# Kernel optimization log

Measured on AMD Instinct MI355X. Metric: run time of the kernel, lower is better.

## Reference

```python
import jax, jax.numpy as jnp
import numpy as np

N = 50000
E = 800000
IN_DIM = 64          # 'in_dim'; ndata h has dim 2*in_dim, p has dim in_dim
EDGE_DIM = 32
OUT_DIM = 64
AVG_D_LOG = 2.8332   # avg_d['log'] = log(avg_degree + 1), avg_degree = 16
EPS_STD = 1e-5
EPS_BN = 1e-5


def setup_inputs() -> dict:
    key = jax.random.key(0)
    ks = jax.random.split(key, 16)
    def glorot(k, fan_in, fan_out):
        lim = np.sqrt(6.0 / (fan_in + fan_out)).astype(np.float32)
        return jax.random.uniform(k, (fan_in, fan_out), jnp.float32, -lim, lim)
    d_pre_h = 2 * 2 * IN_DIM + EDGE_DIM   # 288
    d_pre_p = 2 * IN_DIM + EDGE_DIM       # 160
    d_post_h = (4 * 3 + 2) * IN_DIM       # 896
    d_post_p = (4 * 3 + 1) * IN_DIM       # 832
    return {
        "h": jax.random.normal(ks[0], (N, 2 * IN_DIM), jnp.float32),
        "p": jax.random.normal(ks[1], (N, IN_DIM), jnp.float32),
        "e": jax.random.normal(ks[2], (E, EDGE_DIM), jnp.float32),
        "src": jax.random.randint(ks[3], (E,), 0, N, jnp.int32),
        "dst": jax.random.randint(ks[4], (E,), 0, N, jnp.int32),
        "snorm_n": jax.random.uniform(ks[5], (N, 1), jnp.float32, 0.05, 1.0),
        "W_pre_h": glorot(ks[6], d_pre_h, IN_DIM),
        "b_pre_h": jnp.zeros((IN_DIM,), jnp.float32),
        "W_pre_p": glorot(ks[7], d_pre_p, IN_DIM),
        "b_pre_p": jnp.zeros((IN_DIM,), jnp.float32),
        "W_post_h": glorot(ks[8], d_post_h, OUT_DIM),
        "b_post_h": jnp.zeros((OUT_DIM,), jnp.float32),
        "W_post_p": glorot(ks[9], d_post_p, OUT_DIM),
        "b_post_p": jnp.zeros((OUT_DIM,), jnp.float32),
        "bn_gamma": jnp.ones((OUT_DIM,), jnp.float32),
        "bn_beta": jnp.zeros((OUT_DIM,), jnp.float32),
    }


def _agg_scale(msg, dst, deg):
    # msg: [E, d] edge messages reduced at dst; PNA aggregators mean/max/min/std
    degc = jnp.maximum(deg, 1.0)
    s = jax.ops.segment_sum(msg, dst, num_segments=N)
    mean = s / degc[:, None]
    sq = jax.ops.segment_sum(msg * msg, dst, num_segments=N) / degc[:, None]
    var = jax.nn.relu(sq - mean * mean)
    std = jnp.sqrt(var + EPS_STD)
    has = (deg > 0)[:, None]
    mx = jnp.where(has, jax.ops.segment_max(msg, dst, num_segments=N), 0.0)
    mn = jnp.where(has, jax.ops.segment_min(msg, dst, num_segments=N), 0.0)
    agg = jnp.concatenate([mean, mx, mn, std], axis=1)  # [N, 4d]
    logd = jnp.where(deg > 0, jnp.log(deg + 1.0), 1.0)
    amp = (logd / AVG_D_LOG)[:, None]
    att = (AVG_D_LOG / logd)[:, None]
    # scalers: identity, amplification, attenuation -> [N, 12d]
    return jnp.concatenate([agg, agg * amp, agg * att], axis=1)


def reference(h, p, e, src, dst, snorm_n,
              W_pre_h, b_pre_h, W_pre_p, b_pre_p,
              W_post_h, b_post_h, W_post_p, b_post_p,
              bn_gamma, bn_beta):
    # pretrans (1-layer MLP == linear) on concatenated edge endpoint features
    z_h = jnp.concatenate([h[src], h[dst], e], axis=1)   # [E, 4*in+edge]
    z_p = jnp.concatenate([p[src], p[dst], e], axis=1)   # [E, 2*in+edge]
    e_for_h = z_h @ W_pre_h + b_pre_h                    # [E, in]
    e_for_p = z_p @ W_pre_p + b_pre_p                    # [E, in]

    deg = jax.ops.segment_sum(jnp.ones((E,), jnp.float32), dst, num_segments=N)
    agg_h = _agg_scale(e_for_h, dst, deg)                # [N, 12*in]
    agg_p = _agg_scale(e_for_p, dst, deg)                # [N, 12*in]

    h_cat = jnp.concatenate([h, agg_h], axis=1)          # [N, 14*in]
    p_cat = jnp.concatenate([p, agg_p], axis=1)          # [N, 13*in]
    h_out = h_cat @ W_post_h + b_post_h                  # [N, out]
    p_out = p_cat @ W_post_p + b_post_p                  # [N, out]

    # graph norm
    h_out = h_out * snorm_n
    # batch norm (training-mode batch statistics, biased variance)
    mu = jnp.mean(h_out, axis=0)
    var = jnp.mean((h_out - mu) ** 2, axis=0)
    h_out = (h_out - mu) / jnp.sqrt(var + EPS_BN) * bn_gamma + bn_beta
    # dropout = identity (eval / p=0)
    return h_out, p_out
```

## Files before the change

kernel.cpp:

```cpp
#include <hip/hip_runtime.h>
#include <hip/hip_bf16.h>
#include <hip/hip_fp16.h>


#define N_NODES 50000
#define N_EDGES 800000
#define NS 3200000
#define AVG_D_LOG 2.8332f

typedef unsigned short u16;
typedef unsigned int u32;
typedef __attribute__((ext_vector_type(8))) short short8;
typedef __attribute__((ext_vector_type(4))) float f32x4;

__device__ __forceinline__ float bflo(u32 u) { return __uint_as_float(u << 16); }
__device__ __forceinline__ float bfhi(u32 u) { return __uint_as_float(u & 0xffff0000u); }
__device__ __forceinline__ float bf2f(u16 u) { return __uint_as_float(((u32)u) << 16); }
__device__ __forceinline__ u16 f2bf(float x) {
  u32 u = __float_as_uint(x);
  return (u16)((u + 0x7fff + ((u >> 16) & 1)) >> 16);
}
__device__ __forceinline__ u16 f2h(float x) { return __half_as_ushort(__float2half(x)); }
__device__ __forceinline__ float hlo(u32 u) { return __half2float(__ushort_as_half((u16)(u & 0xffffu))); }
__device__ __forceinline__ float hhi(u32 u) { return __half2float(__ushort_as_half((u16)(u >> 16))); }

__device__ __forceinline__ int is_bf(const void* gamma) {
  return ((const u32*)gamma)[0] == 0x3F803F80u ? 1 : 0;
}

__device__ __forceinline__ f32x4 mfma16(short8 a, short8 b, f32x4 c) {
  return __builtin_amdgcn_mfma_f32_16x16x32_bf16(a, b, c, 0, 0, 0);
}

__device__ __forceinline__ void load8(float z[8], const void* base, size_t off,
                                      int bf) {
  if (bf) {
    uint4 u = *(const uint4*)((const u16*)base + off);
    z[0] = bflo(u.x); z[1] = bfhi(u.x); z[2] = bflo(u.y); z[3] = bfhi(u.y);
    z[4] = bflo(u.z); z[5] = bfhi(u.z); z[6] = bflo(u.w); z[7] = bfhi(u.w);
  } else {
    const float* f = (const float*)base + off;
    float4 a = *(const float4*)f;
    float4 b = *(const float4*)(f + 4);
    z[0] = a.x; z[1] = a.y; z[2] = a.z; z[3] = a.w;
    z[4] = b.x; z[5] = b.y; z[6] = b.z; z[7] = b.w;
  }
}

__device__ __forceinline__ float load1(const void* base, size_t off, int bf) {
  return bf ? bf2f(((const u16*)base)[off]) : ((const float*)base)[off];
}

__device__ __forceinline__ short8 cvt8bf(const float z[8]) {
  union { __hip_bfloat162 b[4]; short8 s; } u;
  u.b[0] = __float22bfloat162_rn(make_float2(z[0], z[1]));
  u.b[1] = __float22bfloat162_rn(make_float2(z[2], z[3]));
  u.b[2] = __float22bfloat162_rn(make_float2(z[4], z[5]));
  u.b[3] = __float22bfloat162_rn(make_float2(z[6], z[7]));
  return u.s;
}

__global__ __launch_bounds__(256) void k_convert(
    const void* __restrict__ Wpreh, const void* __restrict__ Wprep,
    const void* __restrict__ Wposth, const void* __restrict__ Wpostp,
    const void* __restrict__ bpreh, const void* __restrict__ bprep,
    const void* __restrict__ bposth, const void* __restrict__ bpostp,
    const void* __restrict__ gamma, float* __restrict__ bias,
    u16* __restrict__ frag) {
  int i = blockIdx.x * 256 + threadIdx.x;
  if (i >= 256 + 139264) return;
  int bf = is_bf(gamma);
  if (i < 256) {
    const void* s = (i < 64) ? bpreh : (i < 128) ? bprep : (i < 192) ? bposth : bpostp;
    bias[i] = load1(s, i & 63, bf);
    return;
  }
  int g = i - 256;
  const void* W; int fidx, rowoff;
  if (g < 8192)        { W = Wpreh;  fidx = g;          rowoff = 0; }
  else if (g < 16384)  { W = Wpreh;  fidx = g - 8192;   rowoff = 128; }
  else if (g < 20480)  { W = Wprep;  fidx = g - 16384;  rowoff = 0; }
  else if (g < 24576)  { W = Wprep;  fidx = g - 20480;  rowoff = 64; }
  else if (g < 81920)  { W = Wposth; fidx = g - 24576;  rowoff = 0; }
  else if (g < 135168) { W = Wpostp; fidx = g - 81920;  rowoff = 0; }
  else if (g < 137216) { W = Wpreh;  fidx = g - 135168; rowoff = 256; }
  else                 { W = Wprep;  fidx = g - 137216; rowoff = 128; }
  int f = fidx;
  int kc = f >> 11, nt = (f >> 9) & 3, lane = (f >> 3) & 63, j = f & 7;
  int k = kc * 32 + (lane >> 4) * 8 + j;
  int n = nt * 16 + (lane & 15);
  frag[g] = f2bf(load1(W, (size_t)(rowoff + k) * 64 + n, bf));
}

__global__ __launch_bounds__(256) void k_hist(const int* __restrict__ dst,
                                              int* __restrict__ cnt) {
  int i = blockIdx.x * 256 + threadIdx.x;
  if (i < N_EDGES) atomicAdd(cnt + dst[i], 1);
}

__global__ __launch_bounds__(1024) void k_scan1(const int* __restrict__ cnt,
                                                int* __restrict__ offs,
                                                int* __restrict__ bsum) {
  __shared__ int buf[1024];
  int t = threadIdx.x;
  int i = blockIdx.x * 1024 + t;
  int v = (i < N_NODES) ? cnt[i] : 0;
  buf[t] = v;
  __syncthreads();
#pragma unroll
  for (int d = 1; d < 1024; d <<= 1) {
    int x = (t >= d) ? buf[t - d] : 0;
    __syncthreads();
    buf[t] += x;
    __syncthreads();
  }
  if (i < N_NODES) offs[i] = buf[t] - v;
  if (t == 1023) bsum[blockIdx.x] = buf[1023];
}
__global__ void k_scan2(const int* __restrict__ bsum, int* __restrict__ boff,
                        int* __restrict__ offs, int nb) {
  if (threadIdx.x == 0 && blockIdx.x == 0) {
    int run = 0;
    for (int b = 0; b < nb; ++b) { boff[b] = run; run += bsum[b]; }
    offs[N_NODES] = run;
  }
}
__global__ __launch_bounds__(256) void k_scan3(int* __restrict__ offs,
                                               const int* __restrict__ boff,
                                               int* __restrict__ cur) {
  int i = blockIdx.x * 256 + threadIdx.x;
  if (i < N_NODES) {
    int v = offs[i] + boff[i >> 10];
    offs[i] = v;
    cur[i] = v;
  }
}

__global__ __launch_bounds__(256) void k_order(const int* __restrict__ src,
                                               const int* __restrict__ dst,
                                               int* __restrict__ cur,
                                               int2* __restrict__ epack) {
  int i = blockIdx.x * 256 + threadIdx.x;
  if (i < N_EDGES) {
    int pos = atomicAdd(cur + dst[i], 1);
    epack[pos] = make_int2(i, src[i]);
  }
}

__global__ __launch_bounds__(256) void k_uproj(
    const void* __restrict__ h, const void* __restrict__ p,
    const float* __restrict__ bias, const u16* __restrict__ frag,
    const void* __restrict__ gamma, u16* __restrict__ Usrc,
    u16* __restrict__ Udst) {
  int wid = (blockIdx.x * 256 + threadIdx.x) >> 6;
  int lane = threadIdx.x & 63;
  if (wid >= 12500) return;
  int part = wid / 3125;
  int node0 = (wid % 3125) * 16;
  int bf = is_bf(gamma);
  const void* feat = (part < 2) ? h : p;
  int pitch = (part < 2) ? 128 : 64;
  int kcn = (part < 2) ? 4 : 2;
  const u16* bfr = frag + (part == 0 ? 0 : part == 1 ? 8192 : part == 2 ? 16384 : 20480);
  u16* U = (part & 1) ? Udst : Usrc;
  int tw = part >> 1;
  int m = lane & 15, quad = lane >> 4;
  f32x4 acc[4];
#pragma unroll
  for (int nt = 0; nt < 4; ++nt) acc[nt] = (f32x4){0.f, 0.f, 0.f, 0.f};
#pragma unroll
  for (int kc = 0; kc < 4; ++kc) {
    if (kc >= kcn) break;
    float z[8];
    load8(z, feat, (size_t)(node0 + m) * pitch + kc * 32 + quad * 8, bf);
    short8 a = cvt8bf(z);
#pragma unroll
    for (int nt = 0; nt < 4; ++nt) {
      short8 b = *(const short8*)(bfr + (size_t)((kc * 4 + nt) * 64 + lane) * 8);
      acc[nt] = mfma16(a, b, acc[nt]);
    }
  }
  const float* bv = (part == 1) ? bias : (part == 3) ? bias + 64 : nullptr;
#pragma unroll
  for (int r = 0; r < 4; ++r) {
    int node = node0 + quad * 4 + r;
#pragma unroll
    for (int nt = 0; nt < 4; ++nt) {
      int col = nt * 16 + m;
      float v = acc[nt][r] + (bv ? bv[col] : 0.f);
      U[(size_t)node * 128 + col * 2 + tw] = f2h(v);
    }
  }
}

template <int BF>
__global__ __launch_bounds__(256, 4) void k_aggf(
    const void* __restrict__ e, const int2* __restrict__ epack,
    const int* __restrict__ offs, const u32* __restrict__ Us32,
    const u32* __restrict__ Ud32, const u16* __restrict__ Wfh,
    const u16* __restrict__ Wfp, const void* __restrict__ gamma,
    u16* __restrict__ Ah, u16* __restrict__ Ap, float* __restrict__ degf) {
  if (is_bf(gamma) != BF) return;
  int n = blockIdx.x * 4 + (threadIdx.x >> 6);
  int lane = threadIdx.x & 63;
  if (n >= N_NODES) return;
  int m = lane & 15, quad = lane >> 4;
  int s = offs[n], epos = offs[n + 1];
  int deg = epos - s;

  short8 bh[4], bp[4];
#pragma unroll
  for (int nt = 0; nt < 4; ++nt) {
    bh[nt] = *(const short8*)(Wfh + (size_t)(nt * 64 + lane) * 8);
    bp[nt] = *(const short8*)(Wfp + (size_t)(nt * 64 + lane) * 8);
  }
  float uhd[4], upd[4];
#pragma unroll
  for (int nt = 0; nt < 4; ++nt) {
    u32 u = Ud32[(size_t)n * 64 + nt * 16 + m];
    uhd[nt] = hlo(u); upd[nt] = hhi(u);
  }
  float hsum[4], hsq[4], hmx[4], hmn[4], psum[4], psq[4], pmx[4], pmn[4];
#pragma unroll
  for (int nt = 0; nt < 4; ++nt) {
    hsum[nt] = hsq[nt] = psum[nt] = psq[nt] = 0.f;
    hmx[nt] = pmx[nt] = -3.4e38f;
    hmn[nt] = pmn[nt] = 3.4e38f;
  }

  int full = deg & ~15;
  int c0 = 0;
  for (; c0 < full; c0 += 16) {
    int eid = epack[s + c0 + m].x;
    int b0 = s + c0 + quad * 4;
    int sce0 = epack[b0].y, sce1 = epack[b0 + 1].y;
    int sce2 = epack[b0 + 2].y, sce3 = epack[b0 + 3].y;
    u32 usv0[4], usv1[4], usv2[4], usv3[4];
#pragma unroll
    for (int nt = 0; nt < 4; ++nt) {
      usv0[nt] = Us32[(size_t)sce0 * 64 + nt * 16 + m];
      usv1[nt] = Us32[(size_t)sce1 * 64 + nt * 16 + m];
      usv2[nt] = Us32[(size_t)sce2 * 64 + nt * 16 + m];
      usv3[nt] = Us32[(size_t)sce3 * 64 + nt * 16 + m];
    }
    short8 a;
    if (BF) {
      a = *(const short8*)((const u16*)e + (size_t)eid * 32 + quad * 8);
    } else {
      float z[8];
      load8(z, e, (size_t)eid * 32 + quad * 8, 0);
      a = cvt8bf(z);
    }
    {
      f32x4 acc[4];
#pragma unroll
      for (int nt = 0; nt < 4; ++nt)
        acc[nt] = mfma16(a, bh[nt], (f32x4){0.f, 0.f, 0.f, 0.f});
#pragma unroll
      for (int nt = 0; nt < 4; ++nt) {
        float w0 = acc[nt][0] + hlo(usv0[nt]);
        float w1 = acc[nt][1] + hlo(usv1[nt]);
        float w2 = acc[nt][2] + hlo(usv2[nt]);
        float w3 = acc[nt][3] + hlo(usv3[nt]);
        hmx[nt] = fmaxf(fmaxf(hmx[nt], w0), fmaxf(fmaxf(w1, w2), w3));
        hmn[nt] = fminf(fminf(hmn[nt], w0), fminf(fminf(w1, w2), w3));
        hsum[nt] += (w0 + w1) + (w2 + w3);
        hsq[nt] = fmaf(w0, w0, fmaf(w1, w1, fmaf(w2, w2, fmaf(w3, w3, hsq[nt]))));
      }
    }
    {
      f32x4 acc[4];
#pragma unroll
      for (int nt = 0; nt < 4; ++nt)
        acc[nt] = mfma16(a, bp[nt], (f32x4){0.f, 0.f, 0.f, 0.f});
#pragma unroll
      for (int nt = 0; nt < 4; ++nt) {
        float w0 = acc[nt][0] + hhi(usv0[nt]);
        float w1 = acc[nt][1] + hhi(usv1[nt]);
        float w2 = acc[nt][2] + hhi(usv2[nt]);
        float w3 = acc[nt][3] + hhi(usv3[nt]);
        pmx[nt] = fmaxf(fmaxf(pmx[nt], w0), fmaxf(fmaxf(w1, w2), w3));
        pmn[nt] = fminf(fminf(pmn[nt], w0), fminf(fminf(w1, w2), w3));
        psum[nt] += (w0 + w1) + (w2 + w3);
        psq[nt] = fmaf(w0, w0, fmaf(w1, w1, fmaf(w2, w2, fmaf(w3, w3, psq[nt]))));
      }
    }
  }
  if (c0 < deg) {
    int im = s + c0 + m; im = im < epos ? im : epos - 1;
    int eid = epack[im].x;
    int b0 = s + c0 + quad * 4;
    int i0 = b0 < epos ? b0 : epos - 1;
    int i1 = b0 + 1 < epos ? b0 + 1 : epos - 1;
    int i2 = b0 + 2 < epos ? b0 + 2 : epos - 1;
    int i3 = b0 + 3 < epos ? b0 + 3 : epos - 1;
    int sce0 = epack[i0].y, sce1 = epack[i1].y;
    int sce2 = epack[i2].y, sce3 = epack[i3].y;
    u32 usv0[4], usv1[4], usv2[4], usv3[4];
#pragma unroll
    for (int nt = 0; nt < 4; ++nt) {
      usv0[nt] = Us32[(size_t)sce0 * 64 + nt * 16 + m];
      usv1[nt] = Us32[(size_t)sce1 * 64 + nt * 16 + m];
      usv2[nt] = Us32[(size_t)sce2 * 64 + nt * 16 + m];
      usv3[nt] = Us32[(size_t)sce3 * 64 + nt * 16 + m];
    }
    short8 a;
    if (BF) {
      a = *(const short8*)((const u16*)e + (size_t)eid * 32 + quad * 8);
    } else {
      float z[8];
      load8(z, e, (size_t)eid * 32 + quad * 8, 0);
      a = cvt8bf(z);
    }
    bool v0 = (c0 + quad * 4 + 0) < deg;
    bool v1 = (c0 + quad * 4 + 1) < deg;
    bool v2 = (c0 + quad * 4 + 2) < deg;
    bool v3 = (c0 + quad * 4 + 3) < deg;
    {
      f32x4 acc[4];
#pragma unroll
      for (int nt = 0; nt < 4; ++nt)
        acc[nt] = mfma16(a, bh[nt], (f32x4){0.f, 0.f, 0.f, 0.f});
#pragma unroll
      for (int nt = 0; nt < 4; ++nt) {
        float w0 = acc[nt][0] + hlo(usv0[nt]);
        float w1 = acc[nt][1] + hlo(usv1[nt]);
        float w2 = acc[nt][2] + hlo(usv2[nt]);
        float w3 = acc[nt][3] + hlo(usv3[nt]);
        hmx[nt] = fmaxf(fmaxf(hmx[nt], w0), fmaxf(fmaxf(w1, w2), w3));
        hmn[nt] = fminf(fminf(hmn[nt], w0), fminf(fminf(w1, w2), w3));
        float z0 = v0 ? w0 : 0.f, z1 = v1 ? w1 : 0.f;
        float z2 = v2 ? w2 : 0.f, z3 = v3 ? w3 : 0.f;
        hsum[nt] += (z0 + z1) + (z2 + z3);
        hsq[nt] = fmaf(z0, z0, fmaf(z1, z1, fmaf(z2, z2, fmaf(z3, z3, hsq[nt]))));
      }
    }
    {
      f32x4 acc[4];
#pragma unroll
      for (int nt = 0; nt < 4; ++nt)
        acc[nt] = mfma16(a, bp[nt], (f32x4){0.f, 0.f, 0.f, 0.f});
#pragma unroll
      for (int nt = 0; nt < 4; ++nt) {
        float w0 = acc[nt][0] + hhi(usv0[nt]);
        float w1 = acc[nt][1] + hhi(usv1[nt]);
        float w2 = acc[nt][2] + hhi(usv2[nt]);
        float w3 = acc[nt][3] + hhi(usv3[nt]);
        pmx[nt] = fmaxf(fmaxf(pmx[nt], w0), fmaxf(fmaxf(w1, w2), w3));
        pmn[nt] = fminf(fminf(pmn[nt], w0), fminf(fminf(w1, w2), w3));
        float z0 = v0 ? w0 : 0.f, z1 = v1 ? w1 : 0.f;
        float z2 = v2 ? w2 : 0.f, z3 = v3 ? w3 : 0.f;
        psum[nt] += (z0 + z1) + (z2 + z3);
        psq[nt] = fmaf(z0, z0, fmaf(z1, z1, fmaf(z2, z2, fmaf(z3, z3, psq[nt]))));
      }
    }
  }

  float dv = (float)deg;
  bool has = deg > 0;
  float inv = has ? 1.f / dv : 1.f;
  if (lane == 0) degf[n] = dv;

#pragma unroll
  for (int nt = 0; nt < 4; ++nt) {
    hsum[nt] += __shfl_xor(hsum[nt], 16); hsum[nt] += __shfl_xor(hsum[nt], 32);
    hsq[nt] += __shfl_xor(hsq[nt], 16);   hsq[nt] += __shfl_xor(hsq[nt], 32);
    hmx[nt] = fmaxf(hmx[nt], __shfl_xor(hmx[nt], 16));
    hmx[nt] = fmaxf(hmx[nt], __shfl_xor(hmx[nt], 32));
    hmn[nt] = fminf(hmn[nt], __shfl_xor(hmn[nt], 16));
    hmn[nt] = fminf(hmn[nt], __shfl_xor(hmn[nt], 32));
    psum[nt] += __shfl_xor(psum[nt], 16); psum[nt] += __shfl_xor(psum[nt], 32);
    psq[nt] += __shfl_xor(psq[nt], 16);   psq[nt] += __shfl_xor(psq[nt], 32);
    pmx[nt] = fmaxf(pmx[nt], __shfl_xor(pmx[nt], 16));
    pmx[nt] = fmaxf(pmx[nt], __shfl_xor(pmx[nt], 32));
    pmn[nt] = fminf(pmn[nt], __shfl_xor(pmn[nt], 16));
    pmn[nt] = fminf(pmn[nt], __shfl_xor(pmn[nt], 32));
  }

#pragma unroll
  for (int nt = 0; nt < 4; ++nt) {
    {
      float mean_w = hsum[nt] * inv;
      float var = fmaf(-mean_w, mean_w, hsq[nt] * inv);
      var = var > 0.f ? var : 0.f;
      float sd = sqrtf(var + 1e-5f);
      float o = quad == 0 ? (has ? mean_w + uhd[nt] : 0.f)
              : quad == 1 ? (has ? hmx[nt] + uhd[nt] : 0.f)
              : quad == 2 ? (has ? hmn[nt] + uhd[nt] : 0.f) : sd;
      Ah[(size_t)n * 256 + quad * 64 + nt * 16 + m] = f2bf(o);
    }
    {
      float mean_w = psum[nt] * inv;
      float var = fmaf(-mean_w, mean_w, psq[nt] * inv);
      var = var > 0.f ? var : 0.f;
      float sd = sqrtf(var + 1e-5f);
      float o = quad == 0 ? (has ? mean_w + upd[nt] : 0.f)
              : quad == 1 ? (has ? pmx[nt] + upd[nt] : 0.f)
              : quad == 2 ? (has ? pmn[nt] + upd[nt] : 0.f) : sd;
      Ap[(size_t)n * 256 + quad * 64 + nt * 16 + m] = f2bf(o);
    }
  }
}

__global__ __launch_bounds__(256) void k_node(
    const void* __restrict__ h, const void* __restrict__ p,
    const u16* __restrict__ Ah, const u16* __restrict__ Ap,
    const void* __restrict__ snorm, const float* __restrict__ degf,
    const u16* __restrict__ BfH, const u16* __restrict__ BfP,
    const float* __restrict__ biasH, const float* __restrict__ biasP,
    const void* __restrict__ gamma, float* __restrict__ outh,
    float* __restrict__ outp) {
  int w = (blockIdx.x * 256 + threadIdx.x) >> 6;
  int lane = threadIdx.x & 63;
  if (w >= N_NODES / 16) return;
  int bf = is_bf(gamma);
  int m = lane & 15, quad = lane >> 4;
  int node0 = w * 16;

  float ampr[4], attr[4];
#pragma unroll
  for (int r = 0; r < 4; ++r) {
    float dv = degf[node0 + quad * 4 + r];
    float logd = (dv > 0.5f) ? logf(dv + 1.f) : 1.f;
    ampr[r] = logd * (1.f / AVG_D_LOG);
    attr[r] = AVG_D_LOG / logd;
  }

  f32x4 accB[4], accA[4], accT[4];
#pragma unroll
  for (int nt = 0; nt < 4; ++nt) {
    accB[nt] = (f32x4){0.f, 0.f, 0.f, 0.f};
    accA[nt] = (f32x4){0.f, 0.f, 0.f, 0.f};
    accT[nt] = (f32x4){0.f, 0.f, 0.f, 0.f};
  }
#pragma unroll 2
  for (int kc = 0; kc < 12; ++kc) {
    short8 a;
    if (kc < 4) {
      float z[8];
      load8(z, h, (size_t)(node0 + m) * 128 + kc * 32 + quad * 8, bf);
      a = cvt8bf(z);
    } else {
      a = *(const short8*)(Ah + (size_t)(node0 + m) * 256 + (kc - 4) * 32 + quad * 8);
    }
#pragma unroll
    for (int nt = 0; nt < 4; ++nt)
      accB[nt] = mfma16(a, *(const short8*)(BfH + (size_t)((kc * 4 + nt) * 64 + lane) * 8), accB[nt]);
    if (kc >= 4) {
      int kk = kc - 4;
#pragma unroll
      for (int nt = 0; nt < 4; ++nt)
        accA[nt] = mfma16(a, *(const short8*)(BfH + 24576 + (size_t)((kk * 4 + nt) * 64 + lane) * 8), accA[nt]);
#pragma unroll
      for (int nt = 0; nt < 4; ++nt)
        accT[nt] = mfma16(a, *(const short8*)(BfH + 40960 + (size_t)((kk * 4 + nt) * 64 + lane) * 8), accT[nt]);
    }
  }
  float bH[4];
#pragma unroll
  for (int nt = 0; nt < 4; ++nt) bH[nt] = biasH[nt * 16 + m];
#pragma unroll
  for (int r = 0; r < 4; ++r) {
    int node = node0 + quad * 4 + r;
    float sn = load1(snorm, node, bf);
#pragma unroll
    for (int nt = 0; nt < 4; ++nt) {
      float v = accB[nt][r] + ampr[r] * accA[nt][r] + attr[r] * accT[nt][r] + bH[nt];
      outh[(size_t)node * 64 + nt * 16 + m] = v * sn;
    }
  }

#pragma unroll
  for (int nt = 0; nt < 4; ++nt) {
    accB[nt] = (f32x4){0.f, 0.f, 0.f, 0.f};
    accA[nt] = (f32x4){0.f, 0.f, 0.f, 0.f};
    accT[nt] = (f32x4){0.f, 0.f, 0.f, 0.f};
  }
#pragma unroll 2
  for (int kc = 0; kc < 10; ++kc) {
    short8 a;
    if (kc < 2) {
      float z[8];
      load8(z, p, (size_t)(node0 + m) * 64 + kc * 32 + quad * 8, bf);
      a = cvt8bf(z);
    } else {
      a = *(const short8*)(Ap + (size_t)(node0 + m) * 256 + (kc - 2) * 32 + quad * 8);
    }
#pragma unroll
    for (int nt = 0; nt < 4; ++nt)
      accB[nt] = mfma16(a, *(const short8*)(BfP + (size_t)((kc * 4 + nt) * 64 + lane) * 8), accB[nt]);
    if (kc >= 2) {
      int kk = kc - 2;
#pragma unroll
      for (int nt = 0; nt < 4; ++nt)
        accA[nt] = mfma16(a, *(const short8*)(BfP + 20480 + (size_t)((kk * 4 + nt) * 64 + lane) * 8), accA[nt]);
#pragma unroll
      for (int nt = 0; nt < 4; ++nt)
        accT[nt] = mfma16(a, *(const short8*)(BfP + 36864 + (size_t)((kk * 4 + nt) * 64 + lane) * 8), accT[nt]);
    }
  }
  float bP[4];
#pragma unroll
  for (int nt = 0; nt < 4; ++nt) bP[nt] = biasP[nt * 16 + m];
#pragma unroll
  for (int r = 0; r < 4; ++r) {
    int node = node0 + quad * 4 + r;
#pragma unroll
    for (int nt = 0; nt < 4; ++nt) {
      float v = accB[nt][r] + ampr[r] * accA[nt][r] + attr[r] * accT[nt][r] + bP[nt];
      outp[(size_t)node * 64 + nt * 16 + m] = v;
    }
  }
}

__global__ __launch_bounds__(256) void k_bnstats(const float* __restrict__ hpre,
                                                 float* __restrict__ bnacc) {
  int j = threadIdx.x & 63;
  float s = 0.0f, q = 0.0f;
  for (int n = blockIdx.x * 4 + (threadIdx.x >> 6); n < N_NODES;
       n += gridDim.x * 4) {
    float x = hpre[(size_t)n * 64 + j];
    s += x; q += x * x;
  }
  __shared__ float ls[256], lq[256];
  ls[threadIdx.x] = s; lq[threadIdx.x] = q;
  __syncthreads();
  if (threadIdx.x < 64) {
    s = ls[threadIdx.x] + ls[threadIdx.x + 64] + ls[threadIdx.x + 128] + ls[threadIdx.x + 192];
    q = lq[threadIdx.x] + lq[threadIdx.x + 64] + lq[threadIdx.x + 128] + lq[threadIdx.x + 192];
    atomicAdd(bnacc + threadIdx.x, s);
    atomicAdd(bnacc + 64 + threadIdx.x, q);
  }
}

__global__ __launch_bounds__(256) void k_bnapply(
    float* __restrict__ outh, const float* __restrict__ bnacc,
    const void* __restrict__ gamma, const void* __restrict__ beta) {
  int i = blockIdx.x * 256 + threadIdx.x;
  if (i >= NS) return;
  int bf = is_bf(gamma);
  int j = i & 63;
  const float invN = 1.0f / (float)N_NODES;
  float mu = bnacc[j] * invN;
  float var = fmaf(-mu, mu, bnacc[64 + j] * invN);
  var = var > 0.0f ? var : 0.0f;
  float sc = load1(gamma, j, bf) * rsqrtf(var + 1e-5f);
  float sh = load1(beta, j, bf) - mu * sc;
  outh[i] = fmaf(outh[i], sc, sh);
}

extern "C" void kernel_launch(void* const* d_in, const int* in_sizes, int n_in,
                              void* d_out, int out_size, void* d_ws,
                              size_t ws_size, hipStream_t stream) {
  const void* h = d_in[0];
  const void* p = d_in[1];
  const void* e = d_in[2];
  const int* src = (const int*)d_in[3];
  const int* dst = (const int*)d_in[4];
  const void* snorm = d_in[5];
  const void* Wpreh = d_in[6];
  const void* bpreh = d_in[7];
  const void* Wprep = d_in[8];
  const void* bprep = d_in[9];
  const void* Wposth = d_in[10];
  const void* bposth = d_in[11];
  const void* Wpostp = d_in[12];
  const void* bpostp = d_in[13];
  const void* gamma = d_in[14];
  const void* beta = d_in[15];

  float* ws = (float*)d_ws;
  u16* Usrc = (u16*)ws;
  u16* Udst = (u16*)(ws + 3200000L);
  u16* Ah = (u16*)(ws + 6400000L);
  u16* Ap = (u16*)(ws + 12800000L);
  int2* epack = (int2*)(ws + 19200000L);
  int* cnt = (int*)(ws + 20800016L);
  int* offs = (int*)(ws + 20850016L);
  float* degf = ws + 20900020L;
  int* cur = (int*)(ws + 20950020L);
  int* bsum = (int*)(ws + 21000020L);
  int* boff = (int*)(ws + 21000084L);
  float* bnacc = ws + 21000148L;
  float* bias = ws + 21000276L;
  u16* frag = (u16*)(ws + 21000532L);

  u16* fragPostH = frag + 24576;
  u16* fragPostP = frag + 81920;
  u16* fragWehF = frag + 135168;
  u16* fragWepF = frag + 137216;

  float* outh = (float*)d_out;
  float* outp = outh + (size_t)NS;

  int bfh = -1;
  if (in_sizes && n_in >= 16) {
    if (in_sizes[0] == 25600000) bfh = 0;
    else if (in_sizes[0] == 12800000) bfh = 1;
  }

  hipMemsetAsync(cnt, 0, N_NODES * sizeof(int), stream);
  hipMemsetAsync(bnacc, 0, 128 * sizeof(float), stream);
  k_convert<<<(256 + 139264 + 255) / 256, 256, 0, stream>>>(
      Wpreh, Wprep, Wposth, Wpostp, bpreh, bprep, bposth, bpostp, gamma, bias,
      frag);
  k_hist<<<(N_EDGES + 255) / 256, 256, 0, stream>>>(dst, cnt);
  const int NB = (N_NODES + 1023) / 1024;
  k_scan1<<<NB, 1024, 0, stream>>>(cnt, offs, bsum);
  k_scan2<<<1, 64, 0, stream>>>(bsum, boff, offs, NB);
  k_scan3<<<(N_NODES + 255) / 256, 256, 0, stream>>>(offs, boff, cur);
  k_order<<<(N_EDGES + 255) / 256, 256, 0, stream>>>(src, dst, cur, epack);
  k_uproj<<<(12500 + 3) / 4, 256, 0, stream>>>(h, p, bias, frag, gamma, Usrc,
                                               Udst);
  if (bfh != 1)
    k_aggf<0><<<(N_NODES + 3) / 4, 256, 0, stream>>>(
        e, epack, offs, (const u32*)Usrc, (const u32*)Udst, fragWehF, fragWepF,
        gamma, Ah, Ap, degf);
  if (bfh != 0)
    k_aggf<1><<<(N_NODES + 3) / 4, 256, 0, stream>>>(
        e, epack, offs, (const u32*)Usrc, (const u32*)Udst, fragWehF, fragWepF,
        gamma, Ah, Ap, degf);
  k_node<<<(N_NODES / 16 + 3) / 4, 256, 0, stream>>>(
      h, p, Ah, Ap, snorm, degf, fragPostH, fragPostP, bias + 128, bias + 192,
      gamma, outh, outp);
  k_bnstats<<<256, 256, 0, stream>>>(outh, bnacc);
  k_bnapply<<<(NS + 255) / 256, 256, 0, stream>>>(outh, bnacc, gamma, beta);
}
```

Measured before the change: 502.9 us.

## Coalesce aggregate stores via permuted post weights, fuse uproj h/p waves, parallel scan2

The aggregation kernel now writes each aggregate row with lane-contiguous addresses instead of a strided quad/column pattern. The post-projection weight rows are permuted at conversion time so the matmul still sees the same semantics. k_uproj now computes the h and p projections in one wave and writes packed half2 pairs directly, halving wave count and removing separate 16-bit scattered stores. The single-thread block-offset scan is replaced with a wavefront shuffle scan.

```diff
diff --git a/kernel.cpp b/kernel.cpp
--- a/kernel.cpp
+++ b/kernel.cpp
@@ -20,7 +20,6 @@
   u32 u = __float_as_uint(x);
   return (u16)((u + 0x7fff + ((u >> 16) & 1)) >> 16);
 }
-__device__ __forceinline__ u16 f2h(float x) { return __half_as_ushort(__float2half(x)); }
 __device__ __forceinline__ float hlo(u32 u) { return __half2float(__ushort_as_half((u16)(u & 0xffffu))); }
 __device__ __forceinline__ float hhi(u32 u) { return __half2float(__ushort_as_half((u16)(u >> 16))); }
 
@@ -58,6 +57,16 @@
   u.b[2] = __float22bfloat162_rn(make_float2(z[4], z[5]));
   u.b[3] = __float22bfloat162_rn(make_float2(z[6], z[7]));
   return u.s;
+}
+
+__device__ __forceinline__ u32 packh2(float a, float b) {
+  union { __half2 h; u32 u; } x;
+  x.h = __float22half2_rn(make_float2(a, b));
+  return x.u;
+}
+
+__device__ __forceinline__ int sem(int o) {
+  return ((o >> 4) & 3) * 64 + (o >> 6) * 16 + (o & 15);
 }
 
 __global__ __launch_bounds__(256) void k_convert(
@@ -76,20 +85,34 @@
     return;
   }
   int g = i - 256;
-  const void* W; int fidx, rowoff;
+  const void* W; int fidx, rowoff, post = 0;
   if (g < 8192)        { W = Wpreh;  fidx = g;          rowoff = 0; }
   else if (g < 16384)  { W = Wpreh;  fidx = g - 8192;   rowoff = 128; }
   else if (g < 20480)  { W = Wprep;  fidx = g - 16384;  rowoff = 0; }
   else if (g < 24576)  { W = Wprep;  fidx = g - 20480;  rowoff = 64; }
-  else if (g < 81920)  { W = Wposth; fidx = g - 24576;  rowoff = 0; }
-  else if (g < 135168) { W = Wpostp; fidx = g - 81920;  rowoff = 0; }
+  else if (g < 81920)  { W = Wposth; fidx = g - 24576;  rowoff = 0; post = 1; }
+  else if (g < 135168) { W = Wpostp; fidx = g - 81920;  rowoff = 0; post = 2; }
   else if (g < 137216) { W = Wpreh;  fidx = g - 135168; rowoff = 256; }
   else                 { W = Wprep;  fidx = g - 137216; rowoff = 128; }
   int f = fidx;
   int kc = f >> 11, nt = (f >> 9) & 3, lane = (f >> 3) & 63, j = f & 7;
   int k = kc * 32 + (lane >> 4) * 8 + j;
   int n = nt * 16 + (lane & 15);
-  frag[g] = f2bf(load1(W, (size_t)(rowoff + k) * 64 + n, bf));
+  int row;
+  if (post == 1) {
+    row = (k < 128) ? k
+        : (k < 384) ? 128 + sem(k - 128)
+        : (k < 640) ? 384 + sem(k - 384)
+                    : 640 + sem(k - 640);
+  } else if (post == 2) {
+    row = (k < 64) ? k
+        : (k < 320) ? 64 + sem(k - 64)
+        : (k < 576) ? 320 + sem(k - 320)
+                    : 576 + sem(k - 576);
+  } else {
+    row = rowoff + k;
+  }
+  frag[g] = f2bf(load1(W, (size_t)row * 64 + n, bf));
 }
 
 __global__ __launch_bounds__(256) void k_hist(const int* __restrict__ dst,
@@ -119,11 +142,16 @@
 }
 __global__ void k_scan2(const int* __restrict__ bsum, int* __restrict__ boff,
                         int* __restrict__ offs, int nb) {
-  if (threadIdx.x == 0 && blockIdx.x == 0) {
-    int run = 0;
-    for (int b = 0; b < nb; ++b) { boff[b] = run; run += bsum[b]; }
-    offs[N_NODES] = run;
-  }
+  int t = threadIdx.x;
+  int own = (t < nb) ? bsum[t] : 0;
+  int v = own;
+#pragma unroll
+  for (int d = 1; d < 64; d <<= 1) {
+    int x = __shfl_up(v, d);
+    if (t >= d) v += x;
+  }
+  if (t < nb) boff[t] = v - own;
+  if (t == nb - 1) offs[N_NODES] = v;
 }
 __global__ __launch_bounds__(256) void k_scan3(int* __restrict__ offs,
                                                const int* __restrict__ boff,
@@ -150,45 +178,55 @@
 __global__ __launch_bounds__(256) void k_uproj(
     const void* __restrict__ h, const void* __restrict__ p,
     const float* __restrict__ bias, const u16* __restrict__ frag,
-    const void* __restrict__ gamma, u16* __restrict__ Usrc,
-    u16* __restrict__ Udst) {
+    const void* __restrict__ gamma, u32* __restrict__ Usrc,
+    u32* __restrict__ Udst) {
   int wid = (blockIdx.x * 256 + threadIdx.x) >> 6;
   int lane = threadIdx.x & 63;
-  if (wid >= 12500) return;
+  if (wid >= 6250) return;
   int part = wid / 3125;
   int node0 = (wid % 3125) * 16;
   int bf = is_bf(gamma);
-  const void* feat = (part < 2) ? h : p;
-  int pitch = (part < 2) ? 128 : 64;
-  int kcn = (part < 2) ? 4 : 2;
-  const u16* bfr = frag + (part == 0 ? 0 : part == 1 ? 8192 : part == 2 ? 16384 : 20480);
-  u16* U = (part & 1) ? Udst : Usrc;
-  int tw = part >> 1;
+  const u16* bfrH = frag + (part ? 8192 : 0);
+  const u16* bfrP = frag + (part ? 20480 : 16384);
+  u32* U = part ? Udst : Usrc;
   int m = lane & 15, quad = lane >> 4;
-  f32x4 acc[4];
-#pragma unroll
-  for (int nt = 0; nt < 4; ++nt) acc[nt] = (f32x4){0.f, 0.f, 0.f, 0.f};
+  f32x4 accH[4], accP[4];
+#pragma unroll
+  for (int nt = 0; nt < 4; ++nt) {
+    accH[nt] = (f32x4){0.f, 0.f, 0.f, 0.f};
+    accP[nt] = (f32x4){0.f, 0.f, 0.f, 0.f};
+  }
 #pragma unroll
   for (int kc = 0; kc < 4; ++kc) {
-    if (kc >= kcn) break;
     float z[8];
-    load8(z, feat, (size_t)(node0 + m) * pitch + kc * 32 + quad * 8, bf);
+    load8(z, h, (size_t)(node0 + m) * 128 + kc * 32 + quad * 8, bf);
     short8 a = cvt8bf(z);
 #pragma unroll
     for (int nt = 0; nt < 4; ++nt) {
-      short8 b = *(const short8*)(bfr + (size_t)((kc * 4 + nt) * 64 + lane) * 8);
-      acc[nt] = mfma16(a, b, acc[nt]);
-    }
-  }
-  const float* bv = (part == 1) ? bias : (part == 3) ? bias + 64 : nullptr;
+      short8 b = *(const short8*)(bfrH + (size_t)((kc * 4 + nt) * 64 + lane) * 8);
+      accH[nt] = mfma16(a, b, accH[nt]);
+    }
+  }
+#pragma unroll
+  for (int kc = 0; kc < 2; ++kc) {
+    float z[8];
+    load8(z, p, (size_t)(node0 + m) * 64 + kc * 32 + quad * 8, bf);
+    short8 a = cvt8bf(z);
+#pragma unroll
+    for (int nt = 0; nt < 4; ++nt) {
+      short8 b = *(const short8*)(bfrP + (size_t)((kc * 4 + nt) * 64 + lane) * 8);
+      accP[nt] = mfma16(a, b, accP[nt]);
+    }
+  }
 #pragma unroll
   for (int r = 0; r < 4; ++r) {
     int node = node0 + quad * 4 + r;
 #pragma unroll
     for (int nt = 0; nt < 4; ++nt) {
       int col = nt * 16 + m;
-      float v = acc[nt][r] + (bv ? bv[col] : 0.f);
-      U[(size_t)node * 128 + col * 2 + tw] = f2h(v);
+      float vh = accH[nt][r] + (part ? bias[col] : 0.f);
+      float vp = accP[nt][r] + (part ? bias[64 + col] : 0.f);
+      U[(size_t)node * 64 + col] = packh2(vh, vp);
     }
   }
 }
@@ -387,7 +425,7 @@
       float o = quad == 0 ? (has ? mean_w + uhd[nt] : 0.f)
               : quad == 1 ? (has ? hmx[nt] + uhd[nt] : 0.f)
               : quad == 2 ? (has ? hmn[nt] + uhd[nt] : 0.f) : sd;
-      Ah[(size_t)n * 256 + quad * 64 + nt * 16 + m] = f2bf(o);
+      Ah[(size_t)n * 256 + nt * 64 + lane] = f2bf(o);
     }
     {
       float mean_w = psum[nt] * inv;
@@ -397,7 +435,7 @@
       float o = quad == 0 ? (has ? mean_w + upd[nt] : 0.f)
               : quad == 1 ? (has ? pmx[nt] + upd[nt] : 0.f)
               : quad == 2 ? (has ? pmn[nt] + upd[nt] : 0.f) : sd;
-      Ap[(size_t)n * 256 + quad * 64 + nt * 16 + m] = f2bf(o);
+      Ap[(size_t)n * 256 + nt * 64 + lane] = f2bf(o);
     }
   }
 }
@@ -570,8 +608,8 @@
   const void* beta = d_in[15];
 
   float* ws = (float*)d_ws;
-  u16* Usrc = (u16*)ws;
-  u16* Udst = (u16*)(ws + 3200000L);
+  u32* Usrc = (u32*)ws;
+  u32* Udst = (u32*)(ws + 3200000L);
   u16* Ah = (u16*)(ws + 6400000L);
   u16* Ap = (u16*)(ws + 12800000L);
   int2* epack = (int2*)(ws + 19200000L);
@@ -610,16 +648,14 @@
   k_scan2<<<1, 64, 0, stream>>>(bsum, boff, offs, NB);
   k_scan3<<<(N_NODES + 255) / 256, 256, 0, stream>>>(offs, boff, cur);
   k_order<<<(N_EDGES + 255) / 256, 256, 0, stream>>>(src, dst, cur, epack);
-  k_uproj<<<(12500 + 3) / 4, 256, 0, stream>>>(h, p, bias, frag, gamma, Usrc,
-                                               Udst);
+  k_uproj<<<(6250 + 3) / 4, 256, 0, stream>>>(h, p, bias, frag, gamma, Usrc,
+                                              Udst);
   if (bfh != 1)
     k_aggf<0><<<(N_NODES + 3) / 4, 256, 0, stream>>>(
-        e, epack, offs, (const u32*)Usrc, (const u32*)Udst, fragWehF, fragWepF,
-        gamma, Ah, Ap, degf);
+        e, epack, offs, Usrc, Udst, fragWehF, fragWepF, gamma, Ah, Ap, degf);
   if (bfh != 0)
     k_aggf<1><<<(N_NODES + 3) / 4, 256, 0, stream>>>(
-        e, epack, offs, (const u32*)Usrc, (const u32*)Udst, fragWehF, fragWepF,
-        gamma, Ah, Ap, degf);
+        e, epack, offs, Usrc, Udst, fragWehF, fragWepF, gamma, Ah, Ap, degf);
   k_node<<<(N_NODES / 16 + 3) / 4, 256, 0, stream>>>(
       h, p, Ah, Ap, snorm, degf, fragPostH, fragPostP, bias + 128, bias + 192,
       gamma, outh, outp);
```

Measured after the change: 503.2 us. About the same (+0.1%).
